# Kernel tuning notes

Measured on AMD Instinct MI355X. Metric: run time of the kernel, lower is better.

Reference implementation:

```python
import jax, jax.numpy as jnp
import numpy as np

N, C, H, W = 4, 64, 64, 64
EPS = 1e-5


def setup_inputs() -> dict:
    key = jax.random.key(0)
    ks = jax.random.split(key, 8)
    f = lambda k, s: jax.random.normal(k, s, dtype=jnp.float32)
    return {
        "low_feats": f(ks[0], (N, C, H, W)),
        "heat0": f(ks[1], (N, C, H, W)),
        "heat1": f(ks[2], (N, C, H, W)),
        # f_query: 1x1 conv + BN(gamma,beta) + ReLU
        "Wq": f(ks[3], (C, C)) * 0.05, "bq": jnp.zeros((C,), jnp.float32),
        "gq": jnp.ones((C,), jnp.float32), "betaq": jnp.zeros((C,), jnp.float32),
        # f_key: 1x1 conv + BN + ReLU
        "Wk": f(ks[4], (C, C)) * 0.05, "bk": jnp.zeros((C,), jnp.float32),
        "gk": jnp.ones((C,), jnp.float32), "betak": jnp.zeros((C,), jnp.float32),
        # f_value: plain 1x1 conv
        "Wv": f(ks[5], (C, C)) * 0.05, "bv": jnp.zeros((C,), jnp.float32),
    }


def _conv1x1(x, Wc, bc):
    # [N,C,H,W] -> [N,O,H,W]
    return jnp.einsum("oc,nchw->nohw", Wc, x) + bc[None, :, None, None]


def _conv_bn_relu(x, Wc, bc, g, beta):
    y = _conv1x1(x, Wc, bc)
    mu = y.mean(axis=(0, 2, 3), keepdims=True)      # batch-stat BN (train mode)
    var = y.var(axis=(0, 2, 3), keepdims=True)
    y = (y - mu) * jax.lax.rsqrt(var + EPS)
    y = y * g[None, :, None, None] + beta[None, :, None, None]
    return jax.nn.relu(y)


def reference(low_feats, heat0, heat1, Wq, bq, gq, betaq, Wk, bk, gk, betak, Wv, bv):
    n, c, h, w = low_feats.shape
    hw = h * w
    query = _conv_bn_relu(low_feats, Wq, bq, gq, betaq).reshape(n, c, hw).transpose(0, 2, 1)  # [N,HW,C]
    keym = _conv_bn_relu(low_feats, Wk, bk, gk, betak).reshape(n, c, hw)                      # [N,C,HW]
    value = _conv1x1(low_feats, Wv, bv).reshape(n, c, hw).transpose(0, 2, 1)                  # [N,HW,C]
    sim = jax.nn.softmax(jnp.einsum("nqc,nck->nqk", query, keym), axis=-1)                    # [N,HW,HW]
    # dual gated value paths share the softmax map: sim@vI + sim@vC == sim@(vI+vC)
    gate = (heat0 + heat1).reshape(n, c, hw).transpose(0, 2, 1)                               # [N,HW,C]
    gated_v = gate * value
    ctx = jnp.einsum("nqk,nkc->nqc", sim, gated_v)                                            # [N,HW,C]
    return ctx.transpose(0, 2, 1).reshape(n, c, h, w)
```

## Files before the change

kernel.cpp:

```cpp
#include <hip/hip_runtime.h>

#define NB 4
#define CC 64
#define HW 4096
#define NT (NB*HW)
#define EPSV 1e-5f
#define LOG2E 1.4426950408889634f

typedef _Float16 f16;
typedef _Float16 half4 __attribute__((ext_vector_type(4)));
typedef _Float16 half8 __attribute__((ext_vector_type(8)));
typedef float   float4v __attribute__((ext_vector_type(4)));

#define NELEM ((size_t)NB*HW*CC)
#define NSLOT 128

#define PART_OFF 512
#define TEN_OFF  264192

__global__ __launch_bounds__(256)
void conv2_kernel(const float* __restrict__ x,
                  const float* __restrict__ h0, const float* __restrict__ h1,
                  const float* __restrict__ Wq, const float* __restrict__ bq,
                  const float* __restrict__ Wk, const float* __restrict__ bk,
                  const float* __restrict__ Wv, const float* __restrict__ bv,
                  float* __restrict__ ws,
                  f16* __restrict__ q, f16* __restrict__ k, f16* __restrict__ gv)
{
    __shared__ float Wl[3][16*CC];
    __shared__ float xs[CC][128];
    const int t    = threadIdx.x;
    const int n    = blockIdx.y;
    const int z    = blockIdx.z;
    const int px0  = blockIdx.x * 128;
    const int lane = t & 63;
    const int grp  = t >> 6;
    const int ocl  = grp * 4;
    const int oc0  = z*16 + ocl;

    ((float4*)Wl[0])[t] = ((const float4*)(Wq + (size_t)z*16*CC))[t];
    ((float4*)Wl[1])[t] = ((const float4*)(Wk + (size_t)z*16*CC))[t];
    ((float4*)Wl[2])[t] = ((const float4*)(Wv + (size_t)z*16*CC))[t];
    for (int i = t; i < CC*32; i += 256) {
        int ic = i >> 5, c4 = i & 31;
        ((float4*)&xs[ic][0])[c4] =
            ((const float4*)(x + ((size_t)n*CC + ic)*HW + px0))[c4];
    }
    __syncthreads();

    float aq[4][2], ak[4][2], av[4][2];
    #pragma unroll
    for (int j = 0; j < 4; ++j) {
        aq[j][0] = aq[j][1] = bq[oc0+j];
        ak[j][0] = ak[j][1] = bk[oc0+j];
        av[j][0] = av[j][1] = bv[oc0+j];
    }

    for (int ic = 0; ic < CC; ic += 4) {
        float2 xv0 = *(float2*)&xs[ic  ][lane*2];
        float2 xv1 = *(float2*)&xs[ic+1][lane*2];
        float2 xv2 = *(float2*)&xs[ic+2][lane*2];
        float2 xv3 = *(float2*)&xs[ic+3][lane*2];
        #pragma unroll
        for (int j = 0; j < 4; ++j) {
            const int row = (ocl+j)*CC + ic;
            float4 wq = *(const float4*)&Wl[0][row];
            float4 wk = *(const float4*)&Wl[1][row];
            float4 wv = *(const float4*)&Wl[2][row];
            aq[j][0] = fmaf(wq.x,xv0.x, fmaf(wq.y,xv1.x, fmaf(wq.z,xv2.x, fmaf(wq.w,xv3.x, aq[j][0]))));
            aq[j][1] = fmaf(wq.x,xv0.y, fmaf(wq.y,xv1.y, fmaf(wq.z,xv2.y, fmaf(wq.w,xv3.y, aq[j][1]))));
            ak[j][0] = fmaf(wk.x,xv0.x, fmaf(wk.y,xv1.x, fmaf(wk.z,xv2.x, fmaf(wk.w,xv3.x, ak[j][0]))));
            ak[j][1] = fmaf(wk.x,xv0.y, fmaf(wk.y,xv1.y, fmaf(wk.z,xv2.y, fmaf(wk.w,xv3.y, ak[j][1]))));
            av[j][0] = fmaf(wv.x,xv0.x, fmaf(wv.y,xv1.x, fmaf(wv.z,xv2.x, fmaf(wv.w,xv3.x, av[j][0]))));
            av[j][1] = fmaf(wv.x,xv0.y, fmaf(wv.y,xv1.y, fmaf(wv.z,xv2.y, fmaf(wv.w,xv3.y, av[j][1]))));
        }
    }

    const int px = px0 + lane*2;
    const size_t base = ((size_t)n*HW + px)*CC + oc0;
    half4 vq0, vq1, vk0, vk1;
    #pragma unroll
    for (int j = 0; j < 4; ++j) {
        vq0[j] = (f16)aq[j][0]; vq1[j] = (f16)aq[j][1];
        vk0[j] = (f16)ak[j][0]; vk1[j] = (f16)ak[j][1];
    }
    *(half4*)&q[base]      = vq0;  *(half4*)&q[base + CC] = vq1;
    *(half4*)&k[base]      = vk0;  *(half4*)&k[base + CC] = vk1;

    #pragma unroll
    for (int j = 0; j < 4; ++j) {
        size_t gi = ((size_t)n*CC + oc0 + j)*HW + px;
        f16 g0 = (f16)((h0[gi]   + h1[gi]  ) * av[j][0]);
        f16 g1 = (f16)((h0[gi+1] + h1[gi+1]) * av[j][1]);
        gv[gi]   = g0;
        gv[gi+1] = g1;
    }

    float* slot = ws + PART_OFF + (size_t)(n*(HW/128) + blockIdx.x)*256;
    #pragma unroll
    for (int j = 0; j < 4; ++j) {
        float v0 = aq[j][0] + aq[j][1];
        float v1 = aq[j][0]*aq[j][0] + aq[j][1]*aq[j][1];
        float v2 = ak[j][0] + ak[j][1];
        float v3 = ak[j][0]*ak[j][0] + ak[j][1]*ak[j][1];
        #pragma unroll
        for (int off = 32; off > 0; off >>= 1) {
            v0 += __shfl_down(v0, off);
            v1 += __shfl_down(v1, off);
            v2 += __shfl_down(v2, off);
            v3 += __shfl_down(v3, off);
        }
        if (lane == 0) {
            slot[      oc0 + j] = v0;
            slot[ 64 + oc0 + j] = v1;
            slot[128 + oc0 + j] = v2;
            slot[192 + oc0 + j] = v3;
        }
    }
}

__global__ __launch_bounds__(256)
void apply_kernel(f16* __restrict__ q, f16* __restrict__ k,
                  const float* __restrict__ ws,
                  const float* __restrict__ gq, const float* __restrict__ betaq,
                  const float* __restrict__ gk, const float* __restrict__ betak)
{
    __shared__ float tot[128];
    __shared__ float sc[CC], sh[CC];
    const int t = threadIdx.x;
    const int tens = blockIdx.y;

    if (t < 128) {
        const float* base = ws + PART_OFF + tens*128 + t;
        float acc = 0.0f;
        #pragma unroll 8
        for (int s = 0; s < NSLOT; ++s) acc += base[(size_t)s*256];
        tot[t] = acc;
    }
    __syncthreads();
    if (t < 64) {
        float mean = tot[t] * (1.0f / NT);
        float var  = tot[64 + t] * (1.0f / NT) - mean*mean;
        if (tens == 0) {
            float s = gq[t] * rsqrtf(var + EPSV);
            sc[t] = s;  sh[t] = betaq[t] - mean*s;
        } else {
            float s = gk[t] * rsqrtf(var + EPSV);
            sc[t] = s * LOG2E;  sh[t] = (betak[t] - mean*s) * LOG2E;
        }
    }
    __syncthreads();

    f16* p = tens ? k : q;
    const size_t e0 = ((size_t)blockIdx.x * 256 + t) * 16;
    const int c0 = (int)(e0 & 63);

    half8 v0 = *(half8*)&p[e0], v1 = *(half8*)&p[e0 + 8];
    half8 o0, o1;
    #pragma unroll
    for (int j = 0; j < 8; ++j) {
        o0[j] = (f16)fmaxf(fmaf(sc[c0+j],   (float)v0[j], sh[c0+j]),   0.0f);
        o1[j] = (f16)fmaxf(fmaf(sc[c0+8+j], (float)v1[j], sh[c0+8+j]), 0.0f);
    }
    *(half8*)&p[e0]     = o0;
    *(half8*)&p[e0 + 8] = o1;
}

__global__ __launch_bounds__(512, 4)
void attn_kernel(const f16* __restrict__ q, const f16* __restrict__ k,
                 const f16* __restrict__ gv, float* __restrict__ out)
{
    __shared__ float Obuf[8][4][256];
    __shared__ float MLbuf[2][8][32];

    const int t    = threadIdx.x;
    const int n    = blockIdx.y;
    const int w    = t >> 6;
    const int lane = t & 63;
    const int m16  = lane & 15;
    const int kb   = lane >> 4;
    const int q0   = blockIdx.x * 32;

    half8 qf[2][2];
    #pragma unroll
    for (int qt = 0; qt < 2; ++qt) {
        const size_t qb = ((size_t)n*HW + q0 + qt*16 + m16)*CC + kb*8;
        qf[qt][0] = *(const half8*)&q[qb];
        qf[qt][1] = *(const half8*)&q[qb + 32];
    }

    const int    kt0   = w * 512;
    const size_t krow  = (size_t)n*HW*CC;
    const size_t gbase = ((size_t)n*CC + m16)*HW;

    half8 khf[2][2];
    half4 gvf[2][4];
    const half4 ones = {(f16)1.f, (f16)1.f, (f16)1.f, (f16)1.f};

#define LOADK(KT) do {                                                        \
    size_t a_ = krow + ((size_t)(KT) + m16)*CC + kb*8;                        \
    khf[0][0] = *(const half8*)&k[a_];                                        \
    khf[0][1] = *(const half8*)&k[a_ + 32];                                   \
    khf[1][0] = *(const half8*)&k[a_ + 16*CC];                                \
    khf[1][1] = *(const half8*)&k[a_ + 16*CC + 32];                           \
} while (0)

#define LOADGV(KT) do {                                                       \
    size_t g_ = gbase + (size_t)(KT) + kb*4;                                  \
    _Pragma("unroll") for (int k2_ = 0; k2_ < 2; ++k2_)                       \
    _Pragma("unroll") for (int ct_ = 0; ct_ < 4; ++ct_)                       \
        gvf[k2_][ct_] = *(const half4*)&gv[g_ + k2_*16 + (size_t)ct_*16*HW];  \
} while (0)

    float4v accO[2][4], accL[2];
    #pragma unroll
    for (int qt = 0; qt < 2; ++qt) {
        #pragma unroll
        for (int ct = 0; ct < 4; ++ct) accO[qt][ct] = (float4v){0.f,0.f,0.f,0.f};
        accL[qt] = (float4v){0.f,0.f,0.f,0.f};
    }
    float m[2] = {-INFINITY,-INFINITY};

#define STEP(KTN_NEXT) do {                                                   \
    float4v accS[2][2];                                                       \
    _Pragma("unroll") for (int qt_ = 0; qt_ < 2; ++qt_)                       \
    _Pragma("unroll") for (int k2_ = 0; k2_ < 2; ++k2_) {                     \
        float4v z_ = {0.f,0.f,0.f,0.f};                                       \
        z_ = __builtin_amdgcn_mfma_f32_16x16x32_f16(khf[k2_][0], qf[qt_][0], z_, 0,0,0); \
        accS[qt_][k2_] = __builtin_amdgcn_mfma_f32_16x16x32_f16(khf[k2_][1], qf[qt_][1], z_, 0,0,0); \
    }                                                                         \
    LOADK(KTN_NEXT);       \
    float mx[2];                                                              \
    _Pragma("unroll") for (int qt_ = 0; qt_ < 2; ++qt_) {                     \
        float v_ = fmaxf(fmaxf(fmaxf(accS[qt_][0][0], accS[qt_][0][1]),       \
                               fmaxf(accS[qt_][0][2], accS[qt_][0][3])),      \
                         fmaxf(fmaxf(accS[qt_][1][0], accS[qt_][1][1]),       \
                               fmaxf(accS[qt_][1][2], accS[qt_][1][3])));     \
        v_ = fmaxf(v_, __shfl_xor(v_, 16));                                   \
        v_ = fmaxf(v_, __shfl_xor(v_, 32));                                   \
        mx[qt_] = v_;                                                         \
    }                                                                         \
    int need_ = (mx[0] > m[0]) | (mx[1] > m[1]);                              \
    if (__any(need_)) {                                                       \
        _Pragma("unroll") for (int qt_ = 0; qt_ < 2; ++qt_) {                 \
            float mn_ = fmaxf(m[qt_], mx[qt_]);                               \
            float al_ = exp2f(m[qt_] - mn_);                                  \
            m[qt_] = mn_;                                                     \
            accL[qt_][0]*=al_; accL[qt_][1]*=al_;                             \
            accL[qt_][2]*=al_; accL[qt_][3]*=al_;                             \
            _Pragma("unroll") for (int ct_ = 0; ct_ < 4; ++ct_) {             \
                accO[qt_][ct_][0]*=al_; accO[qt_][ct_][1]*=al_;               \
                accO[qt_][ct_][2]*=al_; accO[qt_][ct_][3]*=al_;               \
            }                                                                 \
        }                                                                     \
    }                                                                         \
    _Pragma("unroll") for (int qt_ = 0; qt_ < 2; ++qt_) {                     \
        float p0 = exp2f(accS[qt_][0][0]-m[qt_]), p1 = exp2f(accS[qt_][0][1]-m[qt_]); \
        float p2 = exp2f(accS[qt_][0][2]-m[qt_]), p3 = exp2f(accS[qt_][0][3]-m[qt_]); \
        float p4 = exp2f(accS[qt_][1][0]-m[qt_]), p5 = exp2f(accS[qt_][1][1]-m[qt_]); \
        float p6 = exp2f(accS[qt_][1][2]-m[qt_]), p7 = exp2f(accS[qt_][1][3]-m[qt_]); \
        half4 pfa, pfb;                                                       \
        pfa[0]=(f16)p0; pfa[1]=(f16)p1; pfa[2]=(f16)p2; pfa[3]=(f16)p3;       \
        pfb[0]=(f16)p4; pfb[1]=(f16)p5; pfb[2]=(f16)p6; pfb[3]=(f16)p7;       \
        accL[qt_] = __builtin_amdgcn_mfma_f32_16x16x16f16(ones, pfa, accL[qt_], 0,0,0); \
        accL[qt_] = __builtin_amdgcn_mfma_f32_16x16x16f16(ones, pfb, accL[qt_], 0,0,0); \
        _Pragma("unroll") for (int ct_ = 0; ct_ < 4; ++ct_) {                 \
            float4v o_ = accO[qt_][ct_];                                      \
            o_ = __builtin_amdgcn_mfma_f32_16x16x16f16(gvf[0][ct_], pfa, o_, 0,0,0); \
            accO[qt_][ct_] = __builtin_amdgcn_mfma_f32_16x16x16f16(gvf[1][ct_], pfb, o_, 0,0,0); \
        }                                                                     \
    }                                                                         \
    LOADGV(KTN_NEXT);       \
} while (0)

    LOADK(kt0);
    LOADGV(kt0);
    for (int i2 = 0; i2 < 16; ++i2) {
        STEP(kt0 + (i2+1)*32);
    }

    if (kb == 0) {
        #pragma unroll
        for (int qt = 0; qt < 2; ++qt) {
            MLbuf[0][w][qt*16 + m16] = m[qt];
            MLbuf[1][w][qt*16 + m16] = accL[qt][0];
        }
    }
    __syncthreads();

    float invL[2];
    #pragma unroll
    for (int qt = 0; qt < 2; ++qt) {
        const int r = qt*16 + m16;
        float M = MLbuf[0][0][r];
        #pragma unroll
        for (int src = 1; src < 8; ++src) M = fmaxf(M, MLbuf[0][src][r]);
        float L = 0.0f;
        #pragma unroll
        for (int src = 0; src < 8; ++src)
            L += MLbuf[1][src][r] * exp2f(MLbuf[0][src][r] - M);
        const float f = exp2f(m[qt] - M);
        #pragma unroll
        for (int ct = 0; ct < 4; ++ct) {
            accO[qt][ct][0] *= f; accO[qt][ct][1] *= f;
            accO[qt][ct][2] *= f; accO[qt][ct][3] *= f;
        }
        invL[qt] = 1.0f / L;
    }

    for (int rd = 0; rd < 2; ++rd) {
        __syncthreads();
        #pragma unroll
        for (int ct = 0; ct < 4; ++ct)
            ((float4*)&Obuf[w][ct][0])[lane] =
                (float4){accO[rd][ct][0], accO[rd][ct][1], accO[rd][ct][2], accO[rd][ct][3]};
        __syncthreads();
        if (w < 4) {
            float4 s = ((float4*)&Obuf[0][w][0])[lane];
            #pragma unroll
            for (int src = 1; src < 8; ++src) {
                float4 v = ((float4*)&Obuf[src][w][0])[lane];
                s.x += v.x; s.y += v.y; s.z += v.z; s.w += v.w;
            }
            const float iv = invL[rd];
            const int chb = w*16 + kb*4;
            const int row = q0 + rd*16 + m16;
            out[((size_t)n*CC + chb + 0)*HW + row] = s.x * iv;
            out[((size_t)n*CC + chb + 1)*HW + row] = s.y * iv;
            out[((size_t)n*CC + chb + 2)*HW + row] = s.z * iv;
            out[((size_t)n*CC + chb + 3)*HW + row] = s.w * iv;
        }
    }
#undef STEP
#undef LOADGV
#undef LOADK
}

extern "C" void kernel_launch(void* const* d_in, const int* in_sizes, int n_in,
                              void* d_out, int out_size, void* d_ws, size_t ws_size,
                              hipStream_t stream)
{
    const float* low   = (const float*)d_in[0];
    const float* h0    = (const float*)d_in[1];
    const float* h1    = (const float*)d_in[2];
    const float* Wq    = (const float*)d_in[3];
    const float* bq    = (const float*)d_in[4];
    const float* gq    = (const float*)d_in[5];
    const float* betaq = (const float*)d_in[6];
    const float* Wk    = (const float*)d_in[7];
    const float* bk    = (const float*)d_in[8];
    const float* gk    = (const float*)d_in[9];
    const float* betak = (const float*)d_in[10];
    const float* Wv    = (const float*)d_in[11];
    const float* bv    = (const float*)d_in[12];

    float* wsf = (float*)d_ws;
    float* out = (float*)d_out;

    f16* q  = (f16*)((char*)d_ws + TEN_OFF);
    f16* k  = q + NELEM;
    f16* gv = k + NELEM;

    conv2_kernel<<<dim3(HW/128, NB, 4), 256, 0, stream>>>(
        low, h0, h1, Wq, bq, Wk, bk, Wv, bv, wsf, q, k, gv);

    apply_kernel<<<dim3((int)(NELEM/(256*16)), 2), 256, 0, stream>>>(
        q, k, wsf, gq, betaq, gk, betak);

    attn_kernel<<<dim3(HW/32, NB), 512, 0, stream>>>(q, k, gv, out);
}
```

Baseline: 192.1 us.

## Double-buffer K loads, lazy max rescale, and VALU row-sum in attention loop

The attention inner loop now double-buffers the K fragments so the next tile's loads are issued before the current score MFMAs, which should hide global load latency better. The online-softmax rescale is skipped unless the new max exceeds the running max by a threshold (lazy rescaling), which cuts branch and rescale work. The row-sum no longer uses extra MFMAs with a ones vector; per-lane scalar adds are reduced with shuffles at the end. The lazy threshold lets unnormalized exponentials grow up to 2^8, which risks fp16 overflow in the P values, and the doubled K fragments raise register pressure.

Result: slower. 214.4 us (+11.6%).

```diff
diff --git a/kernel.cpp b/kernel.cpp
--- a/kernel.cpp
+++ b/kernel.cpp
@@ -6,6 +6,7 @@
 #define NT (NB*HW)
 #define EPSV 1e-5f
 #define LOG2E 1.4426950408889634f
+#define THRV 8.0f
 
 typedef _Float16 f16;
 typedef _Float16 half4 __attribute__((ext_vector_type(4)));
@@ -193,16 +194,15 @@
     const size_t krow  = (size_t)n*HW*CC;
     const size_t gbase = ((size_t)n*CC + m16)*HW;
 
-    half8 khf[2][2];
+    half8 khf[2][2][2];
     half4 gvf[2][4];
-    const half4 ones = {(f16)1.f, (f16)1.f, (f16)1.f, (f16)1.f};
-
-#define LOADK(KT) do {                                                        \
+
+#define LOADK(DST, KT) do {                                                   \
     size_t a_ = krow + ((size_t)(KT) + m16)*CC + kb*8;                        \
-    khf[0][0] = *(const half8*)&k[a_];                                        \
-    khf[0][1] = *(const half8*)&k[a_ + 32];                                   \
-    khf[1][0] = *(const half8*)&k[a_ + 16*CC];                                \
-    khf[1][1] = *(const half8*)&k[a_ + 16*CC + 32];                           \
+    khf[DST][0][0] = *(const half8*)&k[a_];                                   \
+    khf[DST][0][1] = *(const half8*)&k[a_ + 32];                              \
+    khf[DST][1][0] = *(const half8*)&k[a_ + 16*CC];                           \
+    khf[DST][1][1] = *(const half8*)&k[a_ + 16*CC + 32];                      \
 } while (0)
 
 #define LOADGV(KT) do {                                                       \
@@ -212,42 +212,40 @@
         gvf[k2_][ct_] = *(const half4*)&gv[g_ + k2_*16 + (size_t)ct_*16*HW];  \
 } while (0)
 
-    float4v accO[2][4], accL[2];
-    #pragma unroll
-    for (int qt = 0; qt < 2; ++qt) {
+    float4v accO[2][4];
+    #pragma unroll
+    for (int qt = 0; qt < 2; ++qt)
         #pragma unroll
         for (int ct = 0; ct < 4; ++ct) accO[qt][ct] = (float4v){0.f,0.f,0.f,0.f};
-        accL[qt] = (float4v){0.f,0.f,0.f,0.f};
-    }
-    float m[2] = {-INFINITY,-INFINITY};
-
-#define STEP(KTN_NEXT) do {                                                   \
+    float accL[2] = {0.f, 0.f};
+    float m[2]    = {-INFINITY,-INFINITY};
+
+#define STEP(B, KTN) do {                                                     \
+    LOADK((B)^1, KTN);     \
     float4v accS[2][2];                                                       \
     _Pragma("unroll") for (int qt_ = 0; qt_ < 2; ++qt_)                       \
     _Pragma("unroll") for (int k2_ = 0; k2_ < 2; ++k2_) {                     \
         float4v z_ = {0.f,0.f,0.f,0.f};                                       \
-        z_ = __builtin_amdgcn_mfma_f32_16x16x32_f16(khf[k2_][0], qf[qt_][0], z_, 0,0,0); \
-        accS[qt_][k2_] = __builtin_amdgcn_mfma_f32_16x16x32_f16(khf[k2_][1], qf[qt_][1], z_, 0,0,0); \
+        z_ = __builtin_amdgcn_mfma_f32_16x16x32_f16(khf[B][k2_][0], qf[qt_][0], z_, 0,0,0); \
+        accS[qt_][k2_] = __builtin_amdgcn_mfma_f32_16x16x32_f16(khf[B][k2_][1], qf[qt_][1], z_, 0,0,0); \
     }                                                                         \
-    LOADK(KTN_NEXT);       \
     float mx[2];                                                              \
     _Pragma("unroll") for (int qt_ = 0; qt_ < 2; ++qt_) {                     \
-        float v_ = fmaxf(fmaxf(fmaxf(accS[qt_][0][0], accS[qt_][0][1]),       \
-                               fmaxf(accS[qt_][0][2], accS[qt_][0][3])),      \
-                         fmaxf(fmaxf(accS[qt_][1][0], accS[qt_][1][1]),       \
-                               fmaxf(accS[qt_][1][2], accS[qt_][1][3])));     \
+        float va_ = fmaxf(fmaxf(accS[qt_][0][0], accS[qt_][0][1]), accS[qt_][0][2]); \
+        float vb_ = fmaxf(fmaxf(accS[qt_][0][3], accS[qt_][1][0]), accS[qt_][1][1]); \
+        float vc_ = fmaxf(fmaxf(accS[qt_][1][2], accS[qt_][1][3]), va_);      \
+        float v_  = fmaxf(vb_, vc_);                                          \
         v_ = fmaxf(v_, __shfl_xor(v_, 16));                                   \
         v_ = fmaxf(v_, __shfl_xor(v_, 32));                                   \
         mx[qt_] = v_;                                                         \
     }                                                                         \
-    int need_ = (mx[0] > m[0]) | (mx[1] > m[1]);                              \
+    int need_ = (mx[0] > m[0] + THRV) | (mx[1] > m[1] + THRV);                \
     if (__any(need_)) {                                                       \
         _Pragma("unroll") for (int qt_ = 0; qt_ < 2; ++qt_) {                 \
             float mn_ = fmaxf(m[qt_], mx[qt_]);                               \
             float al_ = exp2f(m[qt_] - mn_);                                  \
             m[qt_] = mn_;                                                     \
-            accL[qt_][0]*=al_; accL[qt_][1]*=al_;                             \
-            accL[qt_][2]*=al_; accL[qt_][3]*=al_;                             \
+            accL[qt_] *= al_;                                                 \
             _Pragma("unroll") for (int ct_ = 0; ct_ < 4; ++ct_) {             \
                 accO[qt_][ct_][0]*=al_; accO[qt_][ct_][1]*=al_;               \
                 accO[qt_][ct_][2]*=al_; accO[qt_][ct_][3]*=al_;               \
@@ -259,31 +257,39 @@
         float p2 = exp2f(accS[qt_][0][2]-m[qt_]), p3 = exp2f(accS[qt_][0][3]-m[qt_]); \
         float p4 = exp2f(accS[qt_][1][0]-m[qt_]), p5 = exp2f(accS[qt_][1][1]-m[qt_]); \
         float p6 = exp2f(accS[qt_][1][2]-m[qt_]), p7 = exp2f(accS[qt_][1][3]-m[qt_]); \
+        accL[qt_] += ((p0+p1)+(p2+p3)) + ((p4+p5)+(p6+p7));                   \
         half4 pfa, pfb;                                                       \
         pfa[0]=(f16)p0; pfa[1]=(f16)p1; pfa[2]=(f16)p2; pfa[3]=(f16)p3;       \
         pfb[0]=(f16)p4; pfb[1]=(f16)p5; pfb[2]=(f16)p6; pfb[3]=(f16)p7;       \
-        accL[qt_] = __builtin_amdgcn_mfma_f32_16x16x16f16(ones, pfa, accL[qt_], 0,0,0); \
-        accL[qt_] = __builtin_amdgcn_mfma_f32_16x16x16f16(ones, pfb, accL[qt_], 0,0,0); \
         _Pragma("unroll") for (int ct_ = 0; ct_ < 4; ++ct_) {                 \
             float4v o_ = accO[qt_][ct_];                                      \
             o_ = __builtin_amdgcn_mfma_f32_16x16x16f16(gvf[0][ct_], pfa, o_, 0,0,0); \
             accO[qt_][ct_] = __builtin_amdgcn_mfma_f32_16x16x16f16(gvf[1][ct_], pfb, o_, 0,0,0); \
         }                                                                     \
     }                                                                         \
-    LOADGV(KTN_NEXT);       \
+    LOADGV(KTN);        \
 } while (0)
 
-    LOADK(kt0);
+    LOADK(0, kt0);
     LOADGV(kt0);
+    #pragma unroll 2
     for (int i2 = 0; i2 < 16; ++i2) {
-        STEP(kt0 + (i2+1)*32);
-    }
-
+        STEP(i2 & 1, kt0 + (i2+1)*32);
+    }
+
+    float lsum[2];
+    #pragma unroll
+    for (int qt = 0; qt < 2; ++qt) {
+        float l = accL[qt];
+        l += __shfl_xor(l, 16);
+        l += __shfl_xor(l, 32);
+        lsum[qt] = l;
+    }
     if (kb == 0) {
         #pragma unroll
         for (int qt = 0; qt < 2; ++qt) {
             MLbuf[0][w][qt*16 + m16] = m[qt];
-            MLbuf[1][w][qt*16 + m16] = accL[qt][0];
+            MLbuf[1][w][qt*16 + m16] = lsum[qt];
         }
     }
     __syncthreads();
```
